# Optimization experiments

Hardware: AMD Instinct MI355X
Metric: run time of the kernel (lower is better)

The kernel has to match this reference:

```python
import jax, jax.numpy as jnp
import numpy as np

NULL = -1.0
HORIZON = 10   # tile(1, 10, 1) in the original
N_REGIONS = 16


def setup_inputs() -> dict:
    key = jax.random.key(0)
    k1, k2, k3 = jax.random.split(key, 3)
    B, T, N, F = 16, 288, 4096, 2
    x = jax.random.uniform(k1, (B, T, N, F), dtype=jnp.float32) * 100.0
    miss = jax.random.uniform(k2, (B, T, N, F)) < 0.05
    x = jnp.where(miss, NULL, x)
    cluster_id = jax.random.randint(k3, (N,), 0, N_REGIONS)
    return {"data_seq": x, "cluster_id": cluster_id}


def reference(data_seq, cluster_id):
    # data_seq: [B, T, N, F] -> take feature 0 -> [B, T, N]
    x = data_seq[..., 0]
    # invalid_to_nan + nan_to_global_avg == replace -1 entries by global mean of valid entries
    valid = x != NULL
    xz = jnp.where(valid, x, 0.0)
    gmean = jnp.sum(xz) / jnp.maximum(jnp.sum(valid.astype(x.dtype)), 1.0)
    x = jnp.where(valid, x, gmean)
    # mean over time, tiled over prediction horizon: [B, HORIZON, N]
    pred_speed = jnp.tile(jnp.mean(x, axis=1, keepdims=True), (1, HORIZON, 1))
    # per-region mean over nodes (fused segment-mean instead of python loop): [B, HORIZON, R]
    counts = jax.ops.segment_sum(jnp.ones((cluster_id.shape[0],), x.dtype),
                                 cluster_id, num_segments=N_REGIONS)      # [R]
    sums = jax.ops.segment_sum(pred_speed.transpose(2, 0, 1),             # [N, B, H]
                               cluster_id, num_segments=N_REGIONS)        # [R, B, H]
    regional = (sums / jnp.maximum(counts, 1.0)[:, None, None]).transpose(1, 2, 0)
    return pred_speed, regional
```

## Files before the change

kernel.cpp:

```cpp
#include <hip/hip_runtime.h>
#include <hip/hip_bf16.h>

#define BB 16
#define TT 288
#define NN 4096
#define FF 2
#define RR 16
#define HH 10
#define TC 4
#define TSTEP (TT / TC)
#define NULLV (-1.0f)

__global__ __launch_bounds__(256) void k_partial(
    const float* __restrict__ x,
    float* __restrict__ psum, int* __restrict__ pcnt,
    float* __restrict__ gsum, unsigned int* __restrict__ gcnt) {
  const int tid = threadIdx.x;
  const int n   = blockIdx.x * 256 + tid;
  const int tc  = blockIdx.y;
  const int b   = blockIdx.z;

  const float* p = x + ((size_t)(b * TT + tc * TSTEP) * NN + n) * FF;
  float s = 0.0f;
  unsigned int c = 0;
#pragma unroll 8
  for (int t = 0; t < TSTEP; ++t) {
    float v = p[(size_t)t * (NN * FF)];
    bool valid = (v != NULLV);
    s += valid ? v : 0.0f;
    c += valid ? 1u : 0u;
  }
  const size_t o = ((size_t)tc * BB + b) * NN + n;
  psum[o] = s;
  pcnt[o] = (int)c;

  float rs = s;
  unsigned int rc = c;
  for (int off = 32; off > 0; off >>= 1) {
    rs += __shfl_down(rs, off);
    rc += __shfl_down(rc, off);
  }
  __shared__ float sh_s[4];
  __shared__ unsigned int sh_c[4];
  const int wid = tid >> 6;
  if ((tid & 63) == 0) { sh_s[wid] = rs; sh_c[wid] = rc; }
  __syncthreads();
  if (tid == 0) {
    float ts = sh_s[0] + sh_s[1] + sh_s[2] + sh_s[3];
    unsigned int tcnt = sh_c[0] + sh_c[1] + sh_c[2] + sh_c[3];
    atomicAdd(gsum, ts);
    atomicAdd(gcnt, tcnt);
  }
}

__global__ __launch_bounds__(256) void k_pred(
    const float* __restrict__ psum, const int* __restrict__ pcnt,
    const float* __restrict__ gsum, const unsigned int* __restrict__ gcnt,
    const int* __restrict__ cluster,
    float* __restrict__ out, float* __restrict__ regsum) {
  const int tid = threadIdx.x;
  const int idx = blockIdx.x * 256 + tid;
  const int b = idx >> 12;
  const int n = idx & (NN - 1);

  float s = 0.0f;
  int c = 0;
#pragma unroll
  for (int tc = 0; tc < TC; ++tc) {
    const size_t o = (size_t)tc * BB * NN + idx;
    s += psum[o];
    c += pcnt[o];
  }
  const float gmean = *gsum / fmaxf((float)(*gcnt), 1.0f);
  const float pred = (s + (float)(TT - c) * gmean) * (1.0f / (float)TT);

#pragma unroll
  for (int h = 0; h < HH; ++h)
    out[(size_t)(b * HH + h) * NN + n] = pred;

  __shared__ float rs[RR];
  if (tid < RR) rs[tid] = 0.0f;
  __syncthreads();
  atomicAdd(&rs[cluster[n]], pred);
  __syncthreads();
  if (tid < RR) atomicAdd(&regsum[b * RR + tid], rs[tid]);
}

__global__ __launch_bounds__(256) void k_final(
    const int* __restrict__ cluster, const float* __restrict__ regsum,
    float* __restrict__ out2) {
  __shared__ unsigned int hist[RR];
  const int tid = threadIdx.x;
  if (tid < RR) hist[tid] = 0u;
  __syncthreads();
  for (int i = tid; i < NN; i += 256) atomicAdd(&hist[cluster[i]], 1u);
  __syncthreads();
  const int b = tid >> 4;
  const int r = tid & 15;
  const float v = regsum[tid] / fmaxf((float)hist[r], 1.0f);
#pragma unroll
  for (int h = 0; h < HH; ++h)
    out2[(size_t)(b * HH + h) * RR + r] = v;
}

extern "C" void kernel_launch(void* const* d_in, const int* in_sizes, int n_in,
                              void* d_out, int out_size, void* d_ws, size_t ws_size,
                              hipStream_t stream) {
  const float* x       = (const float*)d_in[0];
  const int*   cluster = (const int*)d_in[1];
  float* out = (float*)d_out;

  float*        gsum   = (float*)d_ws;
  unsigned int* gcnt   = (unsigned int*)d_ws + 1;
  float*        regsum = (float*)d_ws + 2;
  float* psum = (float*)((char*)d_ws + 4096);
  int*   pcnt = (int*)((char*)d_ws + 4096 + (size_t)TC * BB * NN * sizeof(float));

  hipMemsetAsync(d_ws, 0, 4096, stream);

  dim3 g1(NN / 256, TC, BB);
  k_partial<<<g1, 256, 0, stream>>>(x, psum, pcnt, gsum, gcnt);

  k_pred<<<(BB * NN) / 256, 256, 0, stream>>>(psum, pcnt, gsum, gcnt, cluster,
                                              out, regsum);

  k_final<<<1, 256, 0, stream>>>(cluster, regsum, out + (size_t)BB * HH * NN);
}
```

Before: 227.1 us.

## Vectorize loads, drop atomics and memset, double time chunks

Each k_partial thread now loads a float4 covering two nodes' (feature0, feature1) pairs and accumulates both, doubling TC to 8 chunks. Per-block partial sums replace the global atomics and the memset, and k_pred reduces the 1024 block partials itself. k_pred and k_final use float4 and per-block regional sums instead of global atomics. The float4 load still brings in the unused feature 1, and every k_pred block redundantly re-reduces the global partials.

```diff
diff --git a/kernel.cpp b/kernel.cpp
--- a/kernel.cpp
+++ b/kernel.cpp
@@ -7,35 +7,37 @@
 #define FF 2
 #define RR 16
 #define HH 10
-#define TC 4
+#define TC 8
 #define TSTEP (TT / TC)
+#define NBLK1 (8 * TC * BB)
 #define NULLV (-1.0f)
 
 __global__ __launch_bounds__(256) void k_partial(
-    const float* __restrict__ x,
-    float* __restrict__ psum, int* __restrict__ pcnt,
-    float* __restrict__ gsum, unsigned int* __restrict__ gcnt) {
+    const float4* __restrict__ x4,
+    float2* __restrict__ psum2, int2* __restrict__ pcnt2,
+    float* __restrict__ bsum, unsigned int* __restrict__ bcnt) {
   const int tid = threadIdx.x;
-  const int n   = blockIdx.x * 256 + tid;
+  const int n0  = blockIdx.x * 512 + tid * 2;
   const int tc  = blockIdx.y;
   const int b   = blockIdx.z;
 
-  const float* p = x + ((size_t)(b * TT + tc * TSTEP) * NN + n) * FF;
-  float s = 0.0f;
-  unsigned int c = 0;
-#pragma unroll 8
+  const float4* p = x4 + ((size_t)(b * TT + tc * TSTEP) * NN + n0) / 2;
+  float s0 = 0.0f, s1 = 0.0f;
+  unsigned int c0 = 0, c1 = 0;
+#pragma unroll 12
   for (int t = 0; t < TSTEP; ++t) {
-    float v = p[(size_t)t * (NN * FF)];
-    bool valid = (v != NULLV);
-    s += valid ? v : 0.0f;
-    c += valid ? 1u : 0u;
+    float4 v = p[(size_t)t * (NN / 2)];
+    bool v0 = (v.x != NULLV);
+    bool v1 = (v.z != NULLV);
+    s0 += v0 ? v.x : 0.0f;  c0 += v0 ? 1u : 0u;
+    s1 += v1 ? v.z : 0.0f;  c1 += v1 ? 1u : 0u;
   }
-  const size_t o = ((size_t)tc * BB + b) * NN + n;
-  psum[o] = s;
-  pcnt[o] = (int)c;
+  const size_t o2 = (((size_t)tc * BB + b) * NN + n0) / 2;
+  psum2[o2] = make_float2(s0, s1);
+  pcnt2[o2] = make_int2((int)c0, (int)c1);
 
-  float rs = s;
-  unsigned int rc = c;
+  float rs = s0 + s1;
+  unsigned int rc = c0 + c1;
   for (int off = 32; off > 0; off >>= 1) {
     rs += __shfl_down(rs, off);
     rc += __shfl_down(rc, off);
@@ -46,48 +48,79 @@
   if ((tid & 63) == 0) { sh_s[wid] = rs; sh_c[wid] = rc; }
   __syncthreads();
   if (tid == 0) {
-    float ts = sh_s[0] + sh_s[1] + sh_s[2] + sh_s[3];
-    unsigned int tcnt = sh_c[0] + sh_c[1] + sh_c[2] + sh_c[3];
-    atomicAdd(gsum, ts);
-    atomicAdd(gcnt, tcnt);
+    const int blk = (blockIdx.z * TC + blockIdx.y) * 8 + blockIdx.x;
+    bsum[blk] = sh_s[0] + sh_s[1] + sh_s[2] + sh_s[3];
+    bcnt[blk] = sh_c[0] + sh_c[1] + sh_c[2] + sh_c[3];
   }
 }
 
 __global__ __launch_bounds__(256) void k_pred(
-    const float* __restrict__ psum, const int* __restrict__ pcnt,
-    const float* __restrict__ gsum, const unsigned int* __restrict__ gcnt,
-    const int* __restrict__ cluster,
-    float* __restrict__ out, float* __restrict__ regsum) {
+    const float4* __restrict__ psum4, const int4* __restrict__ pcnt4,
+    const float4* __restrict__ bsum4, const uint4* __restrict__ bcnt4,
+    const int4* __restrict__ cluster4,
+    float4* __restrict__ out4, float* __restrict__ rsB) {
   const int tid = threadIdx.x;
-  const int idx = blockIdx.x * 256 + tid;
-  const int b = idx >> 12;
-  const int n = idx & (NN - 1);
+  const int blk = blockIdx.x;
+  const int b   = blk >> 2;
+  const int n0  = (blk & 3) * 1024 + tid * 4;
 
-  float s = 0.0f;
-  int c = 0;
+  float4 bs = bsum4[tid];
+  uint4  bc = bcnt4[tid];
+  float rs = bs.x + bs.y + bs.z + bs.w;
+  unsigned int rc = bc.x + bc.y + bc.z + bc.w;
+  for (int off = 32; off > 0; off >>= 1) {
+    rs += __shfl_down(rs, off);
+    rc += __shfl_down(rc, off);
+  }
+  __shared__ float sh_s[4];
+  __shared__ unsigned int sh_c[4];
+  __shared__ float sh_gmean;
+  const int wid = tid >> 6;
+  if ((tid & 63) == 0) { sh_s[wid] = rs; sh_c[wid] = rc; }
+  __syncthreads();
+  if (tid == 0) {
+    float gs = sh_s[0] + sh_s[1] + sh_s[2] + sh_s[3];
+    float gc = (float)(sh_c[0] + sh_c[1] + sh_c[2] + sh_c[3]);
+    sh_gmean = gs / fmaxf(gc, 1.0f);
+  }
+  __syncthreads();
+  const float gmean = sh_gmean;
+
+  float4 s = make_float4(0.f, 0.f, 0.f, 0.f);
+  int4 c = make_int4(0, 0, 0, 0);
 #pragma unroll
   for (int tc = 0; tc < TC; ++tc) {
-    const size_t o = (size_t)tc * BB * NN + idx;
-    s += psum[o];
-    c += pcnt[o];
+    const size_t o4 = (((size_t)tc * BB + b) * NN + n0) / 4;
+    float4 ps = psum4[o4];
+    int4   pc = pcnt4[o4];
+    s.x += ps.x; s.y += ps.y; s.z += ps.z; s.w += ps.w;
+    c.x += pc.x; c.y += pc.y; c.z += pc.z; c.w += pc.w;
   }
-  const float gmean = *gsum / fmaxf((float)(*gcnt), 1.0f);
-  const float pred = (s + (float)(TT - c) * gmean) * (1.0f / (float)TT);
+  const float inv_t = 1.0f / (float)TT;
+  float4 pred;
+  pred.x = (s.x + (float)(TT - c.x) * gmean) * inv_t;
+  pred.y = (s.y + (float)(TT - c.y) * gmean) * inv_t;
+  pred.z = (s.z + (float)(TT - c.z) * gmean) * inv_t;
+  pred.w = (s.w + (float)(TT - c.w) * gmean) * inv_t;
 
 #pragma unroll
   for (int h = 0; h < HH; ++h)
-    out[(size_t)(b * HH + h) * NN + n] = pred;
+    out4[((size_t)(b * HH + h) * NN + n0) / 4] = pred;
 
-  __shared__ float rs[RR];
-  if (tid < RR) rs[tid] = 0.0f;
+  __shared__ float rsh[RR];
+  if (tid < RR) rsh[tid] = 0.0f;
   __syncthreads();
-  atomicAdd(&rs[cluster[n]], pred);
+  int4 cl = cluster4[n0 / 4];
+  atomicAdd(&rsh[cl.x], pred.x);
+  atomicAdd(&rsh[cl.y], pred.y);
+  atomicAdd(&rsh[cl.z], pred.z);
+  atomicAdd(&rsh[cl.w], pred.w);
   __syncthreads();
-  if (tid < RR) atomicAdd(&regsum[b * RR + tid], rs[tid]);
+  if (tid < RR) rsB[blk * RR + tid] = rsh[tid];
 }
 
 __global__ __launch_bounds__(256) void k_final(
-    const int* __restrict__ cluster, const float* __restrict__ regsum,
+    const int* __restrict__ cluster, const float* __restrict__ rsB,
     float* __restrict__ out2) {
   __shared__ unsigned int hist[RR];
   const int tid = threadIdx.x;
@@ -97,7 +130,10 @@
   __syncthreads();
   const int b = tid >> 4;
   const int r = tid & 15;
-  const float v = regsum[tid] / fmaxf((float)hist[r], 1.0f);
+  float s = 0.0f;
+#pragma unroll
+  for (int q = 0; q < 4; ++q) s += rsB[((b << 2) + q) * RR + r];
+  const float v = s / fmaxf((float)hist[r], 1.0f);
 #pragma unroll
   for (int h = 0; h < HH; ++h)
     out2[(size_t)(b * HH + h) * RR + r] = v;
@@ -110,19 +146,19 @@
   const int*   cluster = (const int*)d_in[1];
   float* out = (float*)d_out;
 
-  float*        gsum   = (float*)d_ws;
-  unsigned int* gcnt   = (unsigned int*)d_ws + 1;
-  float*        regsum = (float*)d_ws + 2;
-  float* psum = (float*)((char*)d_ws + 4096);
-  int*   pcnt = (int*)((char*)d_ws + 4096 + (size_t)TC * BB * NN * sizeof(float));
+  float*        psum = (float*)d_ws;
+  int*          pcnt = (int*)((char*)d_ws + (size_t)TC * BB * NN * 4);
+  float*        bsum = (float*)((char*)d_ws + (size_t)2 * TC * BB * NN * 4);
+  unsigned int* bcnt = (unsigned int*)((char*)bsum + 4096);
+  float*        rsB  = (float*)((char*)bsum + 8192);
 
-  hipMemsetAsync(d_ws, 0, 4096, stream);
+  dim3 g1(NN / 512, TC, BB);
+  k_partial<<<g1, 256, 0, stream>>>((const float4*)x, (float2*)psum,
+                                    (int2*)pcnt, bsum, bcnt);
 
-  dim3 g1(NN / 256, TC, BB);
-  k_partial<<<g1, 256, 0, stream>>>(x, psum, pcnt, gsum, gcnt);
+  k_pred<<<64, 256, 0, stream>>>((const float4*)psum, (const int4*)pcnt,
+                                 (const float4*)bsum, (const uint4*)bcnt,
+                                 (const int4*)cluster, (float4*)out, rsB);
 
-  k_pred<<<(BB * NN) / 256, 256, 0, stream>>>(psum, pcnt, gsum, gcnt, cluster,
-                                              out, regsum);
-
-  k_final<<<1, 256, 0, stream>>>(cluster, regsum, out + (size_t)BB * HH * NN);
+  k_final<<<1, 256, 0, stream>>>(cluster, rsB, out + (size_t)BB * HH * NN);
 }
```

New measurement: 216.4 us. 1.05x faster.

## Fuse three kernels into one persistent kernel with flag-based grid sync

Applied to the files above, without the earlier changes.

Replaces the partial-sum, prediction and regional-mean kernels with one kernel of 256 blocks. The blocks exchange per-block sums through release/acquire flags instead of separate launches, global atomics and a memset. Loads now read float4 (two nodes per thread, both features), which halves the number of load instructions but still brings the unused feature 1 into cache. The design depends on all 256 blocks being resident at once. It also relies on MAGIC flags that are never reset between calls, so a later call can see stale flags from an earlier run and read old data.

```diff
diff --git a/kernel.cpp b/kernel.cpp
--- a/kernel.cpp
+++ b/kernel.cpp
@@ -4,103 +4,132 @@
 #define BB 16
 #define TT 288
 #define NN 4096
-#define FF 2
 #define RR 16
 #define HH 10
-#define TC 4
-#define TSTEP (TT / TC)
+#define THALF (TT / 2)
+#define GX (NN / 256)
+#define NBLK (GX * BB)
 #define NULLV (-1.0f)
+#define MAGIC 0x5F17C0DEu
 
-__global__ __launch_bounds__(256) void k_partial(
-    const float* __restrict__ x,
-    float* __restrict__ psum, int* __restrict__ pcnt,
-    float* __restrict__ gsum, unsigned int* __restrict__ gcnt) {
-  const int tid = threadIdx.x;
-  const int n   = blockIdx.x * 256 + tid;
-  const int tc  = blockIdx.y;
-  const int b   = blockIdx.z;
+__device__ __forceinline__ void rel_store_u(unsigned int* p, unsigned int v) {
+  __hip_atomic_store(p, v, __ATOMIC_RELEASE, __HIP_MEMORY_SCOPE_AGENT);
+}
+__device__ __forceinline__ unsigned int acq_load_u(const unsigned int* p) {
+  return __hip_atomic_load(p, __ATOMIC_ACQUIRE, __HIP_MEMORY_SCOPE_AGENT);
+}
+__device__ __forceinline__ void rel_store_f(float* p, float v) {
+  __hip_atomic_store(p, v, __ATOMIC_RELEASE, __HIP_MEMORY_SCOPE_AGENT);
+}
+__device__ __forceinline__ float acq_load_f(const float* p) {
+  return __hip_atomic_load(p, __ATOMIC_ACQUIRE, __HIP_MEMORY_SCOPE_AGENT);
+}
 
-  const float* p = x + ((size_t)(b * TT + tc * TSTEP) * NN + n) * FF;
-  float s = 0.0f;
-  unsigned int c = 0;
+__global__ __launch_bounds__(256) void k_fused(
+    const float4* __restrict__ x4, const int* __restrict__ cluster,
+    float* __restrict__ out, float* __restrict__ out2,
+    float* __restrict__ bsum, float* __restrict__ bcntf,
+    float* __restrict__ rsB,
+    unsigned int* __restrict__ flag1, unsigned int* __restrict__ flag2) {
+  const int tid  = threadIdx.x;
+  const int gx   = blockIdx.x;
+  const int b    = blockIdx.y;
+  const int blk  = b * GX + gx;
+  const int half = tid >> 7;
+  const int tl   = tid & 127;
+  const int n0   = gx * 256 + tl * 2;
+
+  __shared__ float shs[4], shc[4];
+  __shared__ float4 comb[128];
+  __shared__ float2 predsh[128];
+  __shared__ float rsh[RR];
+  __shared__ float sh_gmean;
+
+  const float4* p = x4 + ((size_t)(b * TT + half * THALF) * NN + n0) / 2;
+  float s0 = 0.f, s1 = 0.f, c0 = 0.f, c1 = 0.f;
 #pragma unroll 8
-  for (int t = 0; t < TSTEP; ++t) {
-    float v = p[(size_t)t * (NN * FF)];
-    bool valid = (v != NULLV);
-    s += valid ? v : 0.0f;
-    c += valid ? 1u : 0u;
+  for (int t = 0; t < THALF; ++t) {
+    float4 v = p[(size_t)t * (NN / 2)];
+    s0 += (v.x != NULLV) ? v.x : 0.f;  c0 += (v.x != NULLV) ? 1.f : 0.f;
+    s1 += (v.z != NULLV) ? v.z : 0.f;  c1 += (v.z != NULLV) ? 1.f : 0.f;
   }
-  const size_t o = ((size_t)tc * BB + b) * NN + n;
-  psum[o] = s;
-  pcnt[o] = (int)c;
 
-  float rs = s;
-  unsigned int rc = c;
-  for (int off = 32; off > 0; off >>= 1) {
+  float rs = s0 + s1, rc = c0 + c1;
+  for (int off = 32; off; off >>= 1) {
     rs += __shfl_down(rs, off);
     rc += __shfl_down(rc, off);
   }
-  __shared__ float sh_s[4];
-  __shared__ unsigned int sh_c[4];
-  const int wid = tid >> 6;
-  if ((tid & 63) == 0) { sh_s[wid] = rs; sh_c[wid] = rc; }
+  if ((tid & 63) == 0) { shs[tid >> 6] = rs; shc[tid >> 6] = rc; }
+  if (half == 1) comb[tl] = make_float4(s0, c0, s1, c1);
   __syncthreads();
   if (tid == 0) {
-    float ts = sh_s[0] + sh_s[1] + sh_s[2] + sh_s[3];
-    unsigned int tcnt = sh_c[0] + sh_c[1] + sh_c[2] + sh_c[3];
-    atomicAdd(gsum, ts);
-    atomicAdd(gcnt, tcnt);
+    bsum[blk]  = shs[0] + shs[1] + shs[2] + shs[3];
+    bcntf[blk] = shc[0] + shc[1] + shc[2] + shc[3];
+    rel_store_u(&flag1[blk], MAGIC);
   }
-}
 
-__global__ __launch_bounds__(256) void k_pred(
-    const float* __restrict__ psum, const int* __restrict__ pcnt,
-    const float* __restrict__ gsum, const unsigned int* __restrict__ gcnt,
-    const int* __restrict__ cluster,
-    float* __restrict__ out, float* __restrict__ regsum) {
-  const int tid = threadIdx.x;
-  const int idx = blockIdx.x * 256 + tid;
-  const int b = idx >> 12;
-  const int n = idx & (NN - 1);
+  while (acq_load_u(&flag1[tid]) != MAGIC) __builtin_amdgcn_s_sleep(2);
+  __syncthreads();
 
-  float s = 0.0f;
-  int c = 0;
+  float gbs = bsum[tid], gbc = bcntf[tid];
+  for (int off = 32; off; off >>= 1) {
+    gbs += __shfl_down(gbs, off);
+    gbc += __shfl_down(gbc, off);
+  }
+  if ((tid & 63) == 0) { shs[tid >> 6] = gbs; shc[tid >> 6] = gbc; }
+  __syncthreads();
+  if (tid == 0)
+    sh_gmean = (shs[0] + shs[1] + shs[2] + shs[3]) /
+               fmaxf(shc[0] + shc[1] + shc[2] + shc[3], 1.f);
+  if (tid < RR) rsh[tid] = 0.f;
+  __syncthreads();
+  const float gmean = sh_gmean;
+
+  if (half == 0) {
+    float4 up = comb[tl];
+    s0 += up.x; c0 += up.y; s1 += up.z; c1 += up.w;
+    const float inv_t = 1.0f / (float)TT;
+    float pred0 = (s0 + ((float)TT - c0) * gmean) * inv_t;
+    float pred1 = (s1 + ((float)TT - c1) * gmean) * inv_t;
+    predsh[tl] = make_float2(pred0, pred1);
+    atomicAdd(&rsh[cluster[n0]], pred0);
+    atomicAdd(&rsh[cluster[n0 + 1]], pred1);
+  }
+  __syncthreads();
+
+  {
+    float2 pr = predsh[tl];
 #pragma unroll
-  for (int tc = 0; tc < TC; ++tc) {
-    const size_t o = (size_t)tc * BB * NN + idx;
-    s += psum[o];
-    c += pcnt[o];
+    for (int h = half * 5; h < half * 5 + 5; ++h)
+      ((float2*)out)[((size_t)(b * HH + h) * NN + n0) / 2] = pr;
   }
-  const float gmean = *gsum / fmaxf((float)(*gcnt), 1.0f);
-  const float pred = (s + (float)(TT - c) * gmean) * (1.0f / (float)TT);
 
+  if (tid < RR) rel_store_f(&rsB[blk * RR + tid], rsh[tid]);
+  __syncthreads();
+  if (tid == 0) rel_store_u(&flag2[blk], MAGIC);
+
+  if (gx == 0) {
+    __shared__ unsigned int hist[RR];
+    __shared__ float vsh[RR];
+    if (tid < RR) hist[tid] = 0u;
+    __syncthreads();
+    for (int i = tid; i < NN; i += 256) atomicAdd(&hist[cluster[i]], 1u);
+    if (tid < GX)
+      while (acq_load_u(&flag2[b * GX + tid]) != MAGIC)
+        __builtin_amdgcn_s_sleep(2);
+    __syncthreads();
+    if (tid < RR) {
+      float s = 0.f;
 #pragma unroll
-  for (int h = 0; h < HH; ++h)
-    out[(size_t)(b * HH + h) * NN + n] = pred;
-
-  __shared__ float rs[RR];
-  if (tid < RR) rs[tid] = 0.0f;
-  __syncthreads();
-  atomicAdd(&rs[cluster[n]], pred);
-  __syncthreads();
-  if (tid < RR) atomicAdd(&regsum[b * RR + tid], rs[tid]);
-}
-
-__global__ __launch_bounds__(256) void k_final(
-    const int* __restrict__ cluster, const float* __restrict__ regsum,
-    float* __restrict__ out2) {
-  __shared__ unsigned int hist[RR];
-  const int tid = threadIdx.x;
-  if (tid < RR) hist[tid] = 0u;
-  __syncthreads();
-  for (int i = tid; i < NN; i += 256) atomicAdd(&hist[cluster[i]], 1u);
-  __syncthreads();
-  const int b = tid >> 4;
-  const int r = tid & 15;
-  const float v = regsum[tid] / fmaxf((float)hist[r], 1.0f);
-#pragma unroll
-  for (int h = 0; h < HH; ++h)
-    out2[(size_t)(b * HH + h) * RR + r] = v;
+      for (int g = 0; g < GX; ++g) s += acq_load_f(&rsB[(b * GX + g) * RR + tid]);
+      vsh[tid] = s / fmaxf((float)hist[tid], 1.f);
+    }
+    __syncthreads();
+    if (tid < HH * RR) {
+      const int h = tid >> 4, r = tid & 15;
+      out2[(size_t)(b * HH + h) * RR + r] = vsh[r];
+    }
+  }
 }
 
 extern "C" void kernel_launch(void* const* d_in, const int* in_sizes, int n_in,
@@ -110,19 +139,14 @@
   const int*   cluster = (const int*)d_in[1];
   float* out = (float*)d_out;
 
-  float*        gsum   = (float*)d_ws;
-  unsigned int* gcnt   = (unsigned int*)d_ws + 1;
-  float*        regsum = (float*)d_ws + 2;
-  float* psum = (float*)((char*)d_ws + 4096);
-  int*   pcnt = (int*)((char*)d_ws + 4096 + (size_t)TC * BB * NN * sizeof(float));
+  float*        bsum  = (float*)d_ws;
+  float*        bcntf = (float*)((char*)d_ws + 1024);
+  float*        rsB   = (float*)((char*)d_ws + 2048);
+  unsigned int* flag1 = (unsigned int*)((char*)d_ws + 18432);
+  unsigned int* flag2 = (unsigned int*)((char*)d_ws + 19456);
 
-  hipMemsetAsync(d_ws, 0, 4096, stream);
-
-  dim3 g1(NN / 256, TC, BB);
-  k_partial<<<g1, 256, 0, stream>>>(x, psum, pcnt, gsum, gcnt);
-
-  k_pred<<<(BB * NN) / 256, 256, 0, stream>>>(psum, pcnt, gsum, gcnt, cluster,
-                                              out, regsum);
-
-  k_final<<<1, 256, 0, stream>>>(cluster, regsum, out + (size_t)BB * HH * NN);
+  dim3 grid(GX, BB);
+  k_fused<<<grid, 256, 0, stream>>>((const float4*)x, cluster,
+                                    out, out + (size_t)BB * HH * NN,
+                                    bsum, bcntf, rsB, flag1, flag2);
 }
```

New measurement: 261.8 us. 1.15x slower.
